# Kernel optimization log

Measured on AMD Instinct MI355X. Metric: run time of the kernel, lower is better.

The kernel has to match this reference:

```python
import jax, jax.numpy as jnp
import numpy as np

ALPHA = 0.2  # LeakyReLU negative slope


def setup_inputs() -> dict:
    key = jax.random.key(0)
    ks = jax.random.split(key, 6)
    B, N, F_IN, F_OUT = 4, 4096, 128, 128
    return {
        "input": jax.random.normal(ks[0], (B, N, F_IN), dtype=jnp.float32),
        "adj": jax.random.uniform(ks[1], (B, N, N), dtype=jnp.float32),
        "W": jax.random.normal(ks[2], (F_IN, F_OUT), dtype=jnp.float32) * (np.sqrt(2.0) / np.sqrt(F_IN)),
        "a1": jax.random.normal(ks[3], (F_OUT, 1), dtype=jnp.float32) * 0.1,
        "a2": jax.random.normal(ks[4], (F_OUT, 1), dtype=jnp.float32) * 0.1,
        "bias": jax.random.normal(ks[5], (N, F_OUT), dtype=jnp.float32) * 0.02,
    }


def reference(input, adj, W, a1, a2, bias):
    # h = X @ W : [B, N, F_out]
    h = jnp.einsum("bnf,fo->bno", input, W)
    # additive attention scores: e[b,i,j] = leakyrelu(f1[b,i] + f2[b,j])
    f1 = h @ a1            # [B, N, 1]
    f2 = h @ a2            # [B, N, 1]
    e = f1 + jnp.swapaxes(f2, 1, 2)        # [B, N, N]
    e = jnp.where(e >= 0, e, ALPHA * e)    # LeakyReLU
    # NOTE: original multiplies adj into scores (not -inf masking) and
    # softmaxes over dim=1 (the first node axis), faithfully reproduced.
    attention = jax.nn.softmax(adj * e, axis=1)  # [B, N, N]
    # dropout p=0 / eval mode -> identity
    h_prime = jnp.einsum("bij,bjo->bio", attention, h) + bias[None, :, :]
    # in_features == out_features -> plain residual
    return h_prime + input
```

## Files before the change

### kernel.cpp

```cpp
#include <hip/hip_runtime.h>
#include <hip/hip_bf16.h>

typedef short short8 __attribute__((ext_vector_type(8)));
typedef float f32x4 __attribute__((ext_vector_type(4)));
typedef unsigned short u16;
typedef u16 u16x4 __attribute__((ext_vector_type(4)));
typedef u16 u16x8 __attribute__((ext_vector_type(8)));

static constexpr float kAlpha = 0.2f;

static __device__ inline u16 f2bf(float f) {
  __hip_bfloat16 h = __float2bfloat16(f);
  return *reinterpret_cast<u16*>(&h);
}
static __device__ inline float bf2f(u16 v) {
  unsigned int u = ((unsigned int)v) << 16;
  return __uint_as_float(u);
}

__global__ __launch_bounds__(256) void k1_hW(const float* __restrict__ X,
                                             const float* __restrict__ W,
                                             u16* __restrict__ hbT) {
  int row0 = blockIdx.x * 8;
  int o = threadIdx.x & 127;
  int g = threadIdx.x >> 7;
  __shared__ float Xs[8][128];
#pragma unroll
  for (int s = 0; s < 4; ++s) {
    int idx = threadIdx.x + s * 256;
    Xs[idx >> 7][idx & 127] = X[(size_t)row0 * 128 + idx];
  }
  __syncthreads();
  float acc[4] = {0.f, 0.f, 0.f, 0.f};
  for (int k = 0; k < 128; ++k) {
    float w = W[k * 128 + o];
#pragma unroll
    for (int s = 0; s < 4; ++s) acc[s] += Xs[g + 2 * s][k] * w;
  }
  int b = row0 >> 12;
  int n0 = row0 & 4095;
#pragma unroll
  for (int s = 0; s < 4; ++s)
    hbT[((size_t)b * 128 + o) * 4096 + n0 + g + 2 * s] = f2bf(acc[s]);
}

__global__ __launch_bounds__(256) void k1b_f(const u16* __restrict__ hbT,
                                             const float* __restrict__ a1,
                                             const float* __restrict__ a2,
                                             float* __restrict__ f1,
                                             float* __restrict__ f2) {
  int idx = blockIdx.x * 256 + threadIdx.x;
  int b = idx >> 12;
  int n = idx & 4095;
  const u16* base = hbT + (size_t)b * 128 * 4096 + n;
  float s1 = 0.f, s2 = 0.f;
  for (int o = 0; o < 128; ++o) {
    float h = bf2f(base[(size_t)o * 4096]);
    s1 += h * a1[o];
    s2 += h * a2[o];
  }
  f1[idx] = s1;
  f2[idx] = s2;
}

__global__ __launch_bounds__(256) void k2_dpart(const float* __restrict__ adj,
                                                const float* __restrict__ f1,
                                                const float* __restrict__ f2,
                                                float* __restrict__ dpart) {
  int bid = blockIdx.x;
  int ic = bid & 31;
  int jt = (bid >> 5) & 15;
  int b = bid >> 9;
  int t = threadIdx.x;
  int c = t & 63, r = t >> 6;
  int j = jt * 256 + c * 4;
  const size_t badj = (size_t)b * 4096 * 4096;
  f32x4 f2v = *reinterpret_cast<const f32x4*>(&f2[b * 4096 + j]);
  const float* f1p = f1 + b * 4096;
  int row0 = ic * 128 + r;
  f32x4 sum = (f32x4){0.f, 0.f, 0.f, 0.f};
#pragma unroll 8
  for (int s = 0; s < 32; ++s) {
    int row = row0 + 4 * s;
    f32x4 a = *reinterpret_cast<const f32x4*>(&adj[badj + (size_t)row * 4096 + j]);
    float f1r = f1p[row];
#pragma unroll
    for (int k = 0; k < 4; ++k) {
      float e = f1r + f2v[k];
      e = e >= 0.f ? e : kAlpha * e;
      sum[k] += __expf(a[k] * e);
    }
  }
  __shared__ f32x4 red[256];
  red[t] = sum;
  __syncthreads();
  if (t < 64) {
    f32x4 tt = red[t] + red[t + 64] + red[t + 128] + red[t + 192];
    *reinterpret_cast<f32x4*>(&dpart[(size_t)(b * 32 + ic) * 4096 + j]) = tt;
  }
}

__global__ __launch_bounds__(256) void k2b_scale(const float* __restrict__ dpart,
                                                 const u16* __restrict__ hbT,
                                                 u16* __restrict__ hs) {
  int bid = blockIdx.x;
  int og = bid & 7;
  int jb = (bid >> 3) & 15;
  int b = bid >> 7;
  int j = jb * 256 + threadIdx.x;
  float s = 0.f;
#pragma unroll
  for (int ic = 0; ic < 32; ++ic) s += dpart[(size_t)(b * 32 + ic) * 4096 + j];
  float rd = 1.0f / s;
  const u16* src = hbT + (size_t)b * 128 * 4096 + j;
  u16* dst = hs + (size_t)b * 128 * 4096 + j;
#pragma unroll 4
  for (int o = og * 16; o < og * 16 + 16; ++o) {
    dst[(size_t)o * 4096] = f2bf(bf2f(src[(size_t)o * 4096]) * rd);
  }
}

#define LROW 72
#define BARRIER()                                      \
  {                                                    \
    asm volatile("s_waitcnt lgkmcnt(0)" ::: "memory"); \
    __builtin_amdgcn_s_barrier();                      \
  }
__global__ __launch_bounds__(512, 4) void k3_out(
    const float* __restrict__ adj, const u16* __restrict__ hs,
    const float* __restrict__ f1, const float* __restrict__ f2,
    const float* __restrict__ bias, const float* __restrict__ input,
    float* __restrict__ out) {
  int bid0 = blockIdx.x;
  int bid = ((bid0 & 7) << 6) | (bid0 >> 3);
  int b = bid >> 7;
  int i0 = (bid & 127) * 32;
  int t = threadIdx.x;
  int lane = t & 63;
  int w = t >> 6;

  __shared__ u16 As[2][32 * LROW];
  __shared__ u16 Bs[2][128 * LROW];

  const size_t badj = (size_t)b * 4096 * 4096;
  const u16* hb = hs + (size_t)b * 128 * 4096;
  const float* f2b = f2 + b * 4096;

  int rr = t >> 4;
  int c0 = (t & 15) * 4;
  int bo = t >> 2;
  int bc0 = (t & 3) * 16;

  float f1v = f1[b * 4096 + i0 + rr];

  int rg = w & 1;
  int ch = w >> 1;
  int l15 = lane & 15;
  int l8 = (lane >> 4) * 8;

  f32x4 acc[2];
#pragma unroll
  for (int n = 0; n < 2; ++n) acc[n] = (f32x4){0.f, 0.f, 0.f, 0.f};

  f32x4 raA, raB, raC, raD;
  f32x4 rfA, rfB, rfC, rfD;
  u16x8 rbA0, rbA1, rbB0, rbB1, rbC0, rbC1, rbD0, rbD1;

#define PREFETCH(S, J0)                                                    \
  {                                                                        \
    int jj = (J0) & 4095;         \
    ra##S = *reinterpret_cast<const f32x4*>(                               \
        adj + badj + (size_t)(i0 + rr) * 4096 + jj + c0);                  \
    rf##S = *reinterpret_cast<const f32x4*>(f2b + jj + c0);                \
    const u16x8* bp =                                                      \
        reinterpret_cast<const u16x8*>(hb + (size_t)bo * 4096 + jj + bc0); \
    rb##S##0 = bp[0];                                                      \
    rb##S##1 = bp[1];                                                      \
  }

#define STORE(S, BUF)                                                    \
  {                                                                      \
    u16x4 pv;                                                            \
    _Pragma("unroll") for (int k = 0; k < 4; ++k) {                      \
      float e = f1v + rf##S[k];                                          \
      e = e >= 0.f ? e : kAlpha * e;                                     \
      pv[k] = f2bf(__expf(ra##S[k] * e));                                \
    }                                                                    \
    *reinterpret_cast<u16x4*>(&As[BUF][rr * LROW + c0]) = pv;            \
    *reinterpret_cast<u16x8*>(&Bs[BUF][bo * LROW + bc0]) = rb##S##0;     \
    *reinterpret_cast<u16x8*>(&Bs[BUF][bo * LROW + bc0 + 8]) = rb##S##1; \
  }

#define DOMFMA(BUF)                                                                \
  {                                                                                \
    _Pragma("unroll") for (int kk = 0; kk < 64; kk += 32) {                        \
      short8 af = *reinterpret_cast<const short8*>(                                \
          &As[BUF][(16 * rg + l15) * LROW + kk + l8]);                             \
      _Pragma("unroll") for (int n = 0; n < 2; ++n) {                              \
        short8 bf = *reinterpret_cast<const short8*>(                              \
            &Bs[BUF][(32 * ch + n * 16 + l15) * LROW + kk + l8]);                  \
        acc[n] = __builtin_amdgcn_mfma_f32_16x16x32_bf16(af, bf, acc[n], 0, 0, 0); \
      }                                                                            \
    }                                                                              \
  }

  PREFETCH(A, 0);
  PREFETCH(B, 64);
  PREFETCH(C, 128);
  PREFETCH(D, 192);

  for (int j0 = 0; j0 < 4096; j0 += 256) {
    STORE(A, 0);
    BARRIER();
    DOMFMA(0);
    PREFETCH(A, j0 + 256);
    STORE(B, 1);
    BARRIER();
    DOMFMA(1);
    PREFETCH(B, j0 + 320);
    STORE(C, 0);
    BARRIER();
    DOMFMA(0);
    PREFETCH(C, j0 + 384);
    STORE(D, 1);
    BARRIER();
    DOMFMA(1);
    PREFETCH(D, j0 + 448);
  }

  int colbase = 32 * ch + l15;
  int rowbase = i0 + rg * 16 + (lane >> 4) * 4;
#pragma unroll
  for (int n = 0; n < 2; ++n) {
    int o = colbase + n * 16;
#pragma unroll
    for (int q = 0; q < 4; ++q) {
      int i = rowbase + q;
      size_t oidx = ((size_t)b * 4096 + i) * 128 + o;
      out[oidx] = acc[n][q] + bias[i * 128 + o] + input[oidx];
    }
  }
}

extern "C" void kernel_launch(void* const* d_in, const int* in_sizes, int n_in,
                              void* d_out, int out_size, void* d_ws, size_t ws_size,
                              hipStream_t stream) {
  const float* input = (const float*)d_in[0];
  const float* adj = (const float*)d_in[1];
  const float* W = (const float*)d_in[2];
  const float* a1 = (const float*)d_in[3];
  const float* a2 = (const float*)d_in[4];
  const float* bias = (const float*)d_in[5];
  float* out = (float*)d_out;

  char* ws = (char*)d_ws;
  u16* hbT = (u16*)(ws);
  float* f1 = (float*)(ws + 4194304);
  float* f2 = (float*)(ws + 4259840);
  float* dpart = (float*)(ws + 4325376);
  u16* hs = (u16*)(ws + 6422528);

  k1_hW<<<2048, 256, 0, stream>>>(input, W, hbT);
  k1b_f<<<64, 256, 0, stream>>>(hbT, a1, a2, f1, f2);
  k2_dpart<<<2048, 256, 0, stream>>>(adj, f1, f2, dpart);
  k2b_scale<<<512, 256, 0, stream>>>(dpart, hbT, hs);
  k3_out<<<512, 512, 0, stream>>>(adj, hs, f1, f2, bias, input, out);
}
```

Before: 144.1 us.

## Shrink k3 output tile to 16 rows and 32-wide k-chunks for higher occupancy

Reworks the fused attention-matmul kernel to compute 16 rows per block with 32-column k-steps and a two-stage register prefetch, doubling the grid and targeting 8 blocks per CU. Each thread now loads single adj/f2 floats and one 8-wide hs vector per step, and each wave issues one MFMA per barrier. The intent is more latency hiding through occupancy and smaller register/LDS footprint, at the cost of halved reuse of hs across rows, more barriers per unit of work, and narrower adj loads.

```diff
diff --git a/kernel.cpp b/kernel.cpp
--- a/kernel.cpp
+++ b/kernel.cpp
@@ -4,7 +4,6 @@
 typedef short short8 __attribute__((ext_vector_type(8)));
 typedef float f32x4 __attribute__((ext_vector_type(4)));
 typedef unsigned short u16;
-typedef u16 u16x4 __attribute__((ext_vector_type(4)));
 typedef u16 u16x8 __attribute__((ext_vector_type(8)));
 
 static constexpr float kAlpha = 0.2f;
@@ -120,125 +119,93 @@
   }
 }
 
-#define LROW 72
+#define LROW 36
 #define BARRIER()                                      \
   {                                                    \
     asm volatile("s_waitcnt lgkmcnt(0)" ::: "memory"); \
     __builtin_amdgcn_s_barrier();                      \
   }
-__global__ __launch_bounds__(512, 4) void k3_out(
+__global__ __launch_bounds__(512, 8) void k3_out(
     const float* __restrict__ adj, const u16* __restrict__ hs,
     const float* __restrict__ f1, const float* __restrict__ f2,
     const float* __restrict__ bias, const float* __restrict__ input,
     float* __restrict__ out) {
   int bid0 = blockIdx.x;
-  int bid = ((bid0 & 7) << 6) | (bid0 >> 3);
-  int b = bid >> 7;
-  int i0 = (bid & 127) * 32;
+  int bid = ((bid0 & 7) << 7) | (bid0 >> 3);
+  int b = bid >> 8;
+  int i0 = (bid & 255) * 16;
   int t = threadIdx.x;
   int lane = t & 63;
-  int w = t >> 6;
-
-  __shared__ u16 As[2][32 * LROW];
+  int ch = t >> 6;
+
+  __shared__ u16 As[2][16 * LROW];
   __shared__ u16 Bs[2][128 * LROW];
 
   const size_t badj = (size_t)b * 4096 * 4096;
   const u16* hb = hs + (size_t)b * 128 * 4096;
   const float* f2b = f2 + b * 4096;
 
-  int rr = t >> 4;
-  int c0 = (t & 15) * 4;
+  int rr = t >> 5;
+  int cc = t & 31;
   int bo = t >> 2;
-  int bc0 = (t & 3) * 16;
+  int bc0 = (t & 3) * 8;
 
   float f1v = f1[b * 4096 + i0 + rr];
 
-  int rg = w & 1;
-  int ch = w >> 1;
   int l15 = lane & 15;
   int l8 = (lane >> 4) * 8;
 
-  f32x4 acc[2];
-#pragma unroll
-  for (int n = 0; n < 2; ++n) acc[n] = (f32x4){0.f, 0.f, 0.f, 0.f};
-
-  f32x4 raA, raB, raC, raD;
-  f32x4 rfA, rfB, rfC, rfD;
-  u16x8 rbA0, rbA1, rbB0, rbB1, rbC0, rbC1, rbD0, rbD1;
-
-#define PREFETCH(S, J0)                                                    \
-  {                                                                        \
-    int jj = (J0) & 4095;         \
-    ra##S = *reinterpret_cast<const f32x4*>(                               \
-        adj + badj + (size_t)(i0 + rr) * 4096 + jj + c0);                  \
-    rf##S = *reinterpret_cast<const f32x4*>(f2b + jj + c0);                \
-    const u16x8* bp =                                                      \
-        reinterpret_cast<const u16x8*>(hb + (size_t)bo * 4096 + jj + bc0); \
-    rb##S##0 = bp[0];                                                      \
-    rb##S##1 = bp[1];                                                      \
-  }
-
-#define STORE(S, BUF)                                                    \
+  f32x4 acc = (f32x4){0.f, 0.f, 0.f, 0.f};
+
+  float raA, raB;
+  float rfA, rfB;
+  u16x8 rbA, rbB;
+
+#define PREFETCH(S, J0)                                                  \
   {                                                                      \
-    u16x4 pv;                                                            \
-    _Pragma("unroll") for (int k = 0; k < 4; ++k) {                      \
-      float e = f1v + rf##S[k];                                          \
-      e = e >= 0.f ? e : kAlpha * e;                                     \
-      pv[k] = f2bf(__expf(ra##S[k] * e));                                \
-    }                                                                    \
-    *reinterpret_cast<u16x4*>(&As[BUF][rr * LROW + c0]) = pv;            \
-    *reinterpret_cast<u16x8*>(&Bs[BUF][bo * LROW + bc0]) = rb##S##0;     \
-    *reinterpret_cast<u16x8*>(&Bs[BUF][bo * LROW + bc0 + 8]) = rb##S##1; \
-  }
-
-#define DOMFMA(BUF)                                                                \
-  {                                                                                \
-    _Pragma("unroll") for (int kk = 0; kk < 64; kk += 32) {                        \
-      short8 af = *reinterpret_cast<const short8*>(                                \
-          &As[BUF][(16 * rg + l15) * LROW + kk + l8]);                             \
-      _Pragma("unroll") for (int n = 0; n < 2; ++n) {                              \
-        short8 bf = *reinterpret_cast<const short8*>(                              \
-            &Bs[BUF][(32 * ch + n * 16 + l15) * LROW + kk + l8]);                  \
-        acc[n] = __builtin_amdgcn_mfma_f32_16x16x32_bf16(af, bf, acc[n], 0, 0, 0); \
-      }                                                                            \
-    }                                                                              \
+    int jj = (J0) & 4095;       \
+    ra##S = adj[badj + (size_t)(i0 + rr) * 4096 + jj + cc];              \
+    rf##S = f2b[jj + cc];                                                \
+    rb##S = *reinterpret_cast<const u16x8*>(hb + (size_t)bo * 4096 + jj + bc0); \
+  }
+
+#define STORE(S, BUF)                                                \
+  {                                                                  \
+    float e = f1v + rf##S;                                           \
+    e = e >= 0.f ? e : kAlpha * e;                                   \
+    As[BUF][rr * LROW + cc] = f2bf(__expf(ra##S * e));               \
+    *reinterpret_cast<u16x8*>(&Bs[BUF][bo * LROW + bc0]) = rb##S;    \
+  }
+
+#define DOMFMA(BUF)                                                          \
+  {                                                                          \
+    short8 af = *reinterpret_cast<const short8*>(&As[BUF][l15 * LROW + l8]); \
+    short8 bf = *reinterpret_cast<const short8*>(                            \
+        &Bs[BUF][(16 * ch + l15) * LROW + l8]);                              \
+    acc = __builtin_amdgcn_mfma_f32_16x16x32_bf16(af, bf, acc, 0, 0, 0);     \
   }
 
   PREFETCH(A, 0);
-  PREFETCH(B, 64);
-  PREFETCH(C, 128);
-  PREFETCH(D, 192);
-
-  for (int j0 = 0; j0 < 4096; j0 += 256) {
+  PREFETCH(B, 32);
+
+  for (int j0 = 0; j0 < 4096; j0 += 64) {
     STORE(A, 0);
     BARRIER();
     DOMFMA(0);
-    PREFETCH(A, j0 + 256);
+    PREFETCH(A, j0 + 64);
     STORE(B, 1);
     BARRIER();
     DOMFMA(1);
-    PREFETCH(B, j0 + 320);
-    STORE(C, 0);
-    BARRIER();
-    DOMFMA(0);
-    PREFETCH(C, j0 + 384);
-    STORE(D, 1);
-    BARRIER();
-    DOMFMA(1);
-    PREFETCH(D, j0 + 448);
-  }
-
-  int colbase = 32 * ch + l15;
-  int rowbase = i0 + rg * 16 + (lane >> 4) * 4;
-#pragma unroll
-  for (int n = 0; n < 2; ++n) {
-    int o = colbase + n * 16;
-#pragma unroll
-    for (int q = 0; q < 4; ++q) {
-      int i = rowbase + q;
-      size_t oidx = ((size_t)b * 4096 + i) * 128 + o;
-      out[oidx] = acc[n][q] + bias[i * 128 + o] + input[oidx];
-    }
+    PREFETCH(B, j0 + 96);
+  }
+
+  int o = 16 * ch + l15;
+  int rowbase = i0 + (lane >> 4) * 4;
+#pragma unroll
+  for (int q = 0; q < 4; ++q) {
+    int i = rowbase + q;
+    size_t oidx = ((size_t)b * 4096 + i) * 128 + o;
+    out[oidx] = acc[q] + bias[i * 128 + o] + input[oidx];
   }
 }
 
@@ -264,5 +231,5 @@
   k1b_f<<<64, 256, 0, stream>>>(hbT, a1, a2, f1, f2);
   k2_dpart<<<2048, 256, 0, stream>>>(adj, f1, f2, dpart);
   k2b_scale<<<512, 256, 0, stream>>>(dpart, hbT, hs);
-  k3_out<<<512, 512, 0, stream>>>(adj, hs, f1, f2, bias, input, out);
-}
+  k3_out<<<1024, 512, 0, stream>>>(adj, hs, f1, f2, bias, input, out);
+}
```

New measurement: 202.3 us. +40.4%, slower.
